# Performance work log

Measured on AMD Instinct MI355X. Metric: run time of the kernel, lower is better.

Reference implementation:

```python
import jax, jax.numpy as jnp
import numpy as np

N = 20000      # nodes
E = 640000     # directed edges
NB = 124       # n_atom_basis
FD = NB + 4    # feature dim after res_embed concat = 128
RBF = 16
CUTOFF = 10.0
NCONV = 3
SCF = FD + 10  # sidechain torsion feature dim = 138

act = jax.nn.silu  # 'swish'

def _w(key, shape, fan_in):
    return jax.random.normal(key, shape, jnp.float32) / np.sqrt(fan_in)

def setup_inputs() -> dict:
    key = jax.random.key(0)
    ks = iter(jax.random.split(key, 64))
    cg_z = jax.random.randint(next(ks), (N,), 0, 25)
    cg_xyz = jax.random.normal(next(ks), (N, 3), jnp.float32) * 4.0
    src = jax.random.randint(next(ks), (E,), 0, N)
    off = jax.random.randint(next(ks), (E,), 1, N)
    dst = (src + off) % N  # no self-loops -> dist > 0
    CG_nbr_list = jnp.stack([src, dst], axis=1)
    mapping = jax.random.randint(next(ks), (N,), 0, N)  # unused by forward
    S = jax.random.normal(next(ks), (N, NB), jnp.float32)
    p = {}
    p['res_embed'] = _w(next(ks), (25, 4), 1.0)
    p['msg_W1'] = _w(next(ks), (NCONV, FD, FD), FD); p['msg_b1'] = jnp.zeros((NCONV, FD))
    p['msg_W2'] = _w(next(ks), (NCONV, FD, FD), FD); p['msg_b2'] = jnp.zeros((NCONV, FD))
    p['dist_W'] = _w(next(ks), (NCONV, RBF, FD), RBF); p['dist_b'] = jnp.zeros((NCONV, FD))
    p['dense_W1'] = _w(next(ks), (NCONV, FD, FD), FD); p['dense_b1'] = jnp.zeros((NCONV, FD))
    p['dense_W2'] = _w(next(ks), (NCONV, FD, FD), FD); p['dense_b2'] = jnp.zeros((NCONV, FD))
    p['bb_dist_emb'] = _w(next(ks), (25, 3), 1.0)
    p['sc_dist_emb'] = _w(next(ks), (25, 10), 1.0)
    p['bba_W1'] = _w(next(ks), (FD, 3), FD); p['bba_b1'] = jnp.zeros((3,))
    p['bba_W2'] = _w(next(ks), (3, 3), 3);  p['bba_b2'] = jnp.zeros((3,))
    p['sca_W1'] = _w(next(ks), (FD, 10), FD); p['sca_b1'] = jnp.zeros((10,))
    p['sca_W2'] = _w(next(ks), (10, 10), 10); p['sca_b2'] = jnp.zeros((10,))
    p['bbt_W1'] = _w(next(ks), (FD + 3, 3), FD + 3); p['bbt_b1'] = jnp.zeros((3,))
    p['bbt_W2'] = _w(next(ks), (3, 3), 3); p['bbt_b2'] = jnp.zeros((3,))
    p['sct_W1'] = _w(next(ks), (NCONV, SCF, SCF), SCF); p['sct_b1'] = jnp.zeros((NCONV, SCF))
    p['sct_W2'] = _w(next(ks), (NCONV, SCF, SCF), SCF); p['sct_b2'] = jnp.zeros((NCONV, SCF))
    p['ft_W1'] = _w(next(ks), (SCF, 10), SCF); p['ft_b1'] = jnp.zeros((10,))
    p['ft_W2'] = _w(next(ks), (10, 10), 10); p['ft_b2'] = jnp.zeros((10,))
    return dict(cg_z=cg_z, cg_xyz=cg_xyz, CG_nbr_list=CG_nbr_list, mapping=mapping, S=S, **p)

def reference(cg_z, cg_xyz, CG_nbr_list, mapping, S, res_embed,
              msg_W1, msg_b1, msg_W2, msg_b2, dist_W, dist_b,
              dense_W1, dense_b1, dense_W2, dense_b2,
              bb_dist_emb, sc_dist_emb,
              bba_W1, bba_b1, bba_W2, bba_b2,
              sca_W1, sca_b1, sca_W2, sca_b2,
              bbt_W1, bbt_b1, bbt_W2, bbt_b2,
              sct_W1, sct_b1, sct_W2, sct_b2,
              ft_W1, ft_b1, ft_W2, ft_b2):
    nbr = CG_nbr_list  # already directed (both i>j and j>i present)
    i_idx, j_idx = nbr[:, 0], nbr[:, 1]
    r_ij = cg_xyz[j_idx] - cg_xyz[i_idx]             # [E,3]
    dist = jnp.linalg.norm(r_ij, axis=-1)            # [E]
    # PaiNN radial basis: sin(n*pi*d/cutoff)/d, n=1..RBF
    n_arr = jnp.arange(1, RBF + 1, dtype=jnp.float32)
    rbf = jnp.sin(dist[:, None] * n_arr * (jnp.pi / CUTOFF)) / dist[:, None]  # [E,RBF]
    env = jnp.where(dist < CUTOFF, 0.5 * (jnp.cos(jnp.pi * dist / CUTOFF) + 1.0), 0.0)[:, None]
    S = jnp.concatenate([S, res_embed[cg_z]], axis=-1)  # [N,FD]
    for i in range(NCONV):
        phi = act(S @ msg_W1[i] + msg_b1[i]) @ msg_W2[i] + msg_b2[i]   # [N,FD]
        w_s = (rbf @ dist_W[i] + dist_b[i]) * env                      # [E,FD]
        msg = phi[j_idx] * w_s                                         # gather + per-edge message
        v = jax.ops.segment_sum(msg, i_idx, num_segments=N)            # scatter-add
        h = act(act(v) @ dense_W1[i] + dense_b1[i]) @ dense_W2[i] + dense_b2[i]
        S = S + h
    bb_angle = act(act(S) @ bba_W1 + bba_b1) @ bba_W2 + bba_b2          # [N,3]
    bbt_in = jnp.concatenate([S, bb_angle], axis=-1)
    bb_torsion = act(act(bbt_in) @ bbt_W1 + bbt_b1) @ bbt_W2 + bbt_b2   # [N,3]
    sc_angle = act(act(S) @ sca_W1 + sca_b1) @ sca_W2 + sca_b2          # [N,10]
    sc_S = jnp.concatenate([S, sc_angle], axis=-1)                      # [N,SCF]
    for i in range(NCONV):
        sc_S = sc_S + (act(act(sc_S) @ sct_W1[i] + sct_b1[i]) @ sct_W2[i] + sct_b2[i])
    sc_torsion = act(act(sc_S) @ ft_W1 + ft_b1) @ ft_W2 + ft_b2         # [N,10]
    bb_dist = bb_dist_emb[cg_z][..., None]                              # [N,3,1]
    sc_dist = sc_dist_emb[cg_z][..., None]                              # [N,10,1]
    ic_bb = jnp.concatenate([bb_dist, bb_angle[..., None], bb_torsion[..., None]], axis=-1)  # [N,3,3]
    ic_sc = jnp.concatenate([sc_dist, sc_angle[..., None], sc_torsion[..., None]], axis=-1)  # [N,10,3]
    ic_recon = jnp.concatenate([ic_bb, ic_sc], axis=-2)                 # [N,13,3]
    return ic_recon
```

## Files before the change

kernel.cpp:

```cpp
#include <hip/hip_runtime.h>
#include <hip/hip_bf16.h>

#define DIV_UP(a,b) (((a)+(b)-1)/(b))

typedef __attribute__((ext_vector_type(8))) short bf16x8;
typedef __attribute__((ext_vector_type(4))) float f32x4;

__device__ __forceinline__ float silu_f(float x) {
    return x / (1.0f + __expf(-x));
}
__device__ __forceinline__ unsigned short f2bf(float x) {
    __hip_bfloat16 h = __float2bfloat16(x);
    return *reinterpret_cast<unsigned short*>(&h);
}
__device__ __forceinline__ float bf2f(unsigned short u) {
    unsigned int v = (unsigned int)u << 16;
    return __uint_as_float(v);
}
__device__ __forceinline__ void split_bf(float x, unsigned short& hi, unsigned short& lo) {
    hi = f2bf(x);
    lo = f2bf(x - bf2f(hi));
}
__device__ __forceinline__ bf16x8 pack8(unsigned int w0, unsigned int w1,
                                        unsigned int w2, unsigned int w3) {
    union { unsigned int u[4]; bf16x8 v; } t;
    t.u[0] = w0; t.u[1] = w1; t.u[2] = w2; t.u[3] = w3;
    return t.v;
}

#define WSLOT 16384

__global__ __launch_bounds__(256) void prep_weights_kernel(
    const float* __restrict__ msgW1, const float* __restrict__ msgW2,
    const float* __restrict__ denseW1, const float* __restrict__ denseW2,
    unsigned short* __restrict__ WB)
{
    int slot = blockIdx.y;
    int kind = slot / 3, conv = slot % 3;
    const float* base;
    switch (kind) {
        case 0: base = msgW1; break;
        case 1: base = msgW2; break;
        case 2: base = denseW1; break;
        default: base = denseW2; break;
    }
    const float* W = base + (size_t)conv * 128 * 128;
    int idx = blockIdx.x * 256 + threadIdx.x;
    if (idx >= 16384) return;
    int c = idx >> 7, k = idx & 127;
    float val = W[(size_t)k * 128 + c];
    unsigned short hi, lo;
    split_bf(val, hi, lo);
    WB[(size_t)(2 * slot) * WSLOT + idx]     = hi;
    WB[(size_t)(2 * slot + 1) * WSLOT + idx] = lo;
}

__global__ __launch_bounds__(256) void hist_kernel(
    const int* __restrict__ nbr, int* __restrict__ counts, int E)
{
    int e = blockIdx.x * 256 + threadIdx.x;
    if (e < E) atomicAdd(&counts[nbr[2 * e]], 1);
}

__global__ __launch_bounds__(1024) void scan_kernel(
    const int* __restrict__ counts, int* __restrict__ peptr, int N)
{
    __shared__ int part[1024];
    const int t = threadIdx.x;
    const int chunk = DIV_UP(N, 1024);
    int s = 0;
    for (int c = 0; c < chunk; ++c) {
        int idx = t * chunk + c;
        if (idx < N) s += (counts[idx] + 31) & ~31;
    }
    part[t] = s;
    __syncthreads();
    for (int off = 1; off < 1024; off <<= 1) {
        int v = (t >= off) ? part[t - off] : 0;
        __syncthreads();
        part[t] += v;
        __syncthreads();
    }
    int pre = (t > 0) ? part[t - 1] : 0;
    for (int c = 0; c < chunk; ++c) {
        int idx = t * chunk + c;
        if (idx < N) { peptr[idx] = pre; pre += (counts[idx] + 31) & ~31; }
    }
    if (t == 1023) peptr[N] = part[1023];
}

__global__ __launch_bounds__(256) void geom_scatter_kernel(
    const int* __restrict__ nbr, const float* __restrict__ xyz,
    const int* __restrict__ peptr, int* __restrict__ cursor,
    unsigned short* __restrict__ rbfT, unsigned short* __restrict__ envs,
    int* __restrict__ js, int E)
{
    int e = blockIdx.x * 256 + threadIdx.x;
    if (e >= E) return;
    int i = nbr[2 * e], j = nbr[2 * e + 1];
    float dx = xyz[3 * j + 0] - xyz[3 * i + 0];
    float dy = xyz[3 * j + 1] - xyz[3 * i + 1];
    float dz = xyz[3 * j + 2] - xyz[3 * i + 2];
    float dist = sqrtf(dx * dx + dy * dy + dz * dz);
    float x = dist * 0.3141592653589793f;
    float s, c;
    __sincosf(x, &s, &c);
    float env = (dist < 10.0f) ? 0.5f * (c + 1.0f) : 0.0f;
    float inv_env = env / dist;
    float two_c = 2.0f * c;
    float sm1 = 0.0f, s0 = s;
    __align__(16) unsigned short ob[16];
    #pragma unroll
    for (int k = 0; k < 16; ++k) {
        ob[k] = f2bf(s0 * inv_env);
        float s1 = two_c * s0 - sm1;
        sm1 = s0; s0 = s1;
    }
    int p = peptr[i] + atomicAdd(&cursor[i], 1);
    uint4* rp = (uint4*)(rbfT + (size_t)p * 16);
    rp[0] = *(const uint4*)&ob[0];
    rp[1] = *(const uint4*)&ob[8];
    envs[p] = f2bf(env);
    js[p] = j;
}

__global__ __launch_bounds__(256) void concat_s_kernel(
    const float* __restrict__ S, const float* __restrict__ res_embed,
    const int* __restrict__ z, float* __restrict__ S0, int N)
{
    int idx = blockIdx.x * 256 + threadIdx.x;
    if (idx >= N * 128) return;
    int n = idx >> 7, c = idx & 127;
    float val = (c < 124) ? S[n * 124 + c] : res_embed[z[n] * 4 + (c - 124)];
    S0[idx] = val;
}

template<int MT, bool PREACT, bool RESID, typename OutT>
__global__ __launch_bounds__(256) void mlp2_mfma_kernel(
    const float* __restrict__ X,
    const unsigned short* __restrict__ W1hi, const unsigned short* __restrict__ W1lo,
    const float* __restrict__ b1,
    const unsigned short* __restrict__ W2hi, const unsigned short* __restrict__ W2lo,
    const float* __restrict__ b2,
    OutT* __restrict__ Y, int nrows)
{
    constexpr int RB   = MT / 16;
    constexpr int ROWB = 256;
    __shared__ __align__(16) unsigned short XHhi[MT * 128];
    __shared__ __align__(16) unsigned short XHlo[MT * 128];
    __shared__ __align__(16) unsigned short WS[128 * 128];

    const int tid  = threadIdx.x;
    const int wave = tid >> 6;
    const int lane = tid & 63;
    const int l15  = lane & 15;
    const int kg   = lane >> 4;
    const int row0 = blockIdx.x * MT;

    for (int idx = tid; idx < MT * 32; idx += 256) {
        int r = idx >> 5, q = idx & 31;
        int gr = row0 + r;
        float4 xv = make_float4(0.f, 0.f, 0.f, 0.f);
        if (gr < nrows) xv = *(const float4*)(X + (size_t)gr * 128 + 4 * q);
        if (PREACT) { xv.x = silu_f(xv.x); xv.y = silu_f(xv.y);
                      xv.z = silu_f(xv.z); xv.w = silu_f(xv.w); }
        ushort4 h, l;
        split_bf(xv.x, h.x, l.x); split_bf(xv.y, h.y, l.y);
        split_bf(xv.z, h.z, l.z); split_bf(xv.w, h.w, l.w);
        int off = (8 * q) ^ ((r & 7) << 4);
        *(ushort4*)((char*)XHhi + r * ROWB + off) = h;
        *(ushort4*)((char*)XHlo + r * ROWB + off) = l;
    }

    f32x4 acc[RB][2];

    #define STAGE_W(WPTR)                                                       \
        for (int idx = tid; idx < 2048; idx += 256) {                           \
            int r = idx >> 4;                                                   \
            int byt = (idx & 15) * 16;                                          \
            *(uint4*)((char*)WS + r * ROWB + (byt ^ ((r & 7) << 4))) =          \
                *(const uint4*)((WPTR) + (size_t)idx * 8);                      \
        }

    #define PASS(WITH_LO)                                                       \
        _Pragma("unroll")                                                       \
        for (int kk = 0; kk < 4; ++kk) {                                        \
            const int kbyte = kk * 64 + kg * 16;                                \
            bf16x8 ah[RB], al[RB];                                              \
            _Pragma("unroll")                                                   \
            for (int rb = 0; rb < RB; ++rb) {                                   \
                int r = 16 * rb + l15;                                          \
                int off = kbyte ^ ((r & 7) << 4);                               \
                ah[rb] = *(const bf16x8*)((const char*)XHhi + r * ROWB + off);  \
                if (WITH_LO)                                                    \
                    al[rb] = *(const bf16x8*)((const char*)XHlo + r * ROWB + off); \
            }                                                                   \
            _Pragma("unroll")                                                   \
            for (int cbi = 0; cbi < 2; ++cbi) {                                 \
                int rw = 16 * (wave + 4 * cbi) + l15;                           \
                int offw = kbyte ^ ((rw & 7) << 4);                             \
                bf16x8 bw = *(const bf16x8*)((const char*)WS + rw * ROWB + offw); \
                _Pragma("unroll")                                               \
                for (int rb = 0; rb < RB; ++rb) {                               \
                    f32x4 t = acc[rb][cbi];                                     \
                    t = __builtin_amdgcn_mfma_f32_16x16x32_bf16(ah[rb], bw, t, 0, 0, 0); \
                    if (WITH_LO)                                                \
                        t = __builtin_amdgcn_mfma_f32_16x16x32_bf16(al[rb], bw, t, 0, 0, 0); \
                    acc[rb][cbi] = t;                                           \
                }                                                               \
            }                                                                   \
        }

    #pragma unroll
    for (int a = 0; a < RB; ++a) { acc[a][0] = (f32x4){0,0,0,0}; acc[a][1] = (f32x4){0,0,0,0}; }
    STAGE_W(W1hi)
    __syncthreads();
    PASS(true)
    __syncthreads();
    STAGE_W(W1lo)
    __syncthreads();
    PASS(false)
    __syncthreads();

    #pragma unroll
    for (int cbi = 0; cbi < 2; ++cbi) {
        int col = 16 * (wave + 4 * cbi) + l15;
        float b1v = b1[col];
        #pragma unroll
        for (int rb = 0; rb < RB; ++rb)
            #pragma unroll
            for (int i = 0; i < 4; ++i) {
                int r = 16 * rb + kg * 4 + i;
                float h = silu_f(acc[rb][cbi][i] + b1v);
                unsigned short hh, hl;
                split_bf(h, hh, hl);
                int off = (2 * col) ^ ((r & 7) << 4);
                *(unsigned short*)((char*)XHhi + r * ROWB + off) = hh;
                *(unsigned short*)((char*)XHlo + r * ROWB + off) = hl;
            }
    }
    #pragma unroll
    for (int a = 0; a < RB; ++a) { acc[a][0] = (f32x4){0,0,0,0}; acc[a][1] = (f32x4){0,0,0,0}; }
    STAGE_W(W2hi)
    __syncthreads();
    PASS(true)
    __syncthreads();
    STAGE_W(W2lo)
    __syncthreads();
    PASS(false)
    #undef PASS
    #undef STAGE_W

    #pragma unroll
    for (int cbi = 0; cbi < 2; ++cbi) {
        int col = 16 * (wave + 4 * cbi) + l15;
        float b2v = b2[col];
        #pragma unroll
        for (int rb = 0; rb < RB; ++rb)
            #pragma unroll
            for (int i = 0; i < 4; ++i) {
                int gr = row0 + 16 * rb + kg * 4 + i;
                if (gr < nrows) {
                    size_t off = (size_t)gr * 128 + col;
                    float val = acc[rb][cbi][i] + b2v;
                    if (RESID) val += (float)Y[off];
                    if constexpr (sizeof(OutT) == 2)
                        Y[off] = __float2bfloat16(val);
                    else
                        Y[off] = val;
                }
            }
    }
}

template<int K, int ROWS, int RR, bool PREACT, bool RESID, typename OutT>
__global__ __launch_bounds__(256) void mlp2_kernel(
    const float* __restrict__ X, int ldX,
    const float* __restrict__ W1, const float* __restrict__ b1,
    const float* __restrict__ W2, const float* __restrict__ b2,
    OutT* __restrict__ Y, int ldY, int nrows)
{
    constexpr int NC = (K + 31) / 32;
    __shared__ float Xs[ROWS * K];
    __shared__ float Hs[ROWS * K];
    const int tid = threadIdx.x;
    const int row0 = blockIdx.x * ROWS;

    for (int idx = tid; idx < ROWS * K; idx += 256) {
        int r = idx / K, c = idx - r * K;
        int gr = row0 + r;
        float x = (gr < nrows) ? X[(size_t)gr * ldX + c] : 0.0f;
        if (PREACT) x = silu_f(x);
        Xs[idx] = x;
    }
    __syncthreads();

    const int cc = tid & 31;
    const int r0 = (tid >> 5) * RR;

    float acc[NC][RR];
    #pragma unroll
    for (int jc = 0; jc < NC; ++jc) {
        int col = cc + 32 * jc;
        float bv = (col < K) ? b1[col] : 0.0f;
        #pragma unroll
        for (int rr = 0; rr < RR; ++rr) acc[jc][rr] = bv;
    }
    #pragma unroll 6
    for (int k = 0; k < K; ++k) {
        float w[NC];
        #pragma unroll
        for (int jc = 0; jc < NC; ++jc) {
            int col = cc + 32 * jc;
            w[jc] = (col < K) ? W1[k * K + col] : 0.0f;
        }
        float xv[RR];
        #pragma unroll
        for (int rr = 0; rr < RR; ++rr) xv[rr] = Xs[(r0 + rr) * K + k];
        #pragma unroll
        for (int jc = 0; jc < NC; ++jc)
            #pragma unroll
            for (int rr = 0; rr < RR; ++rr)
                acc[jc][rr] = fmaf(xv[rr], w[jc], acc[jc][rr]);
    }
    #pragma unroll
    for (int jc = 0; jc < NC; ++jc) {
        int col = cc + 32 * jc;
        if (col < K) {
            #pragma unroll
            for (int rr = 0; rr < RR; ++rr)
                Hs[(r0 + rr) * K + col] = silu_f(acc[jc][rr]);
        }
    }
    __syncthreads();

    #pragma unroll
    for (int jc = 0; jc < NC; ++jc) {
        int col = cc + 32 * jc;
        float bv = (col < K) ? b2[col] : 0.0f;
        #pragma unroll
        for (int rr = 0; rr < RR; ++rr) acc[jc][rr] = bv;
    }
    #pragma unroll 6
    for (int k = 0; k < K; ++k) {
        float w[NC];
        #pragma unroll
        for (int jc = 0; jc < NC; ++jc) {
            int col = cc + 32 * jc;
            w[jc] = (col < K) ? W2[k * K + col] : 0.0f;
        }
        float xv[RR];
        #pragma unroll
        for (int rr = 0; rr < RR; ++rr) xv[rr] = Hs[(r0 + rr) * K + k];
        #pragma unroll
        for (int jc = 0; jc < NC; ++jc)
            #pragma unroll
            for (int rr = 0; rr < RR; ++rr)
                acc[jc][rr] = fmaf(xv[rr], w[jc], acc[jc][rr]);
    }
    #pragma unroll
    for (int jc = 0; jc < NC; ++jc) {
        int col = cc + 32 * jc;
        if (col < K) {
            #pragma unroll
            for (int rr = 0; rr < RR; ++rr) {
                int gr = row0 + r0 + rr;
                if (gr < nrows) {
                    size_t off = (size_t)gr * ldY + col;
                    float val = acc[jc][rr];
                    if (RESID) val += (float)Y[off];
                    if constexpr (sizeof(OutT) == 2)
                        Y[off] = __float2bfloat16(val);
                    else
                        Y[off] = val;
                }
            }
        }
    }
}

__global__ __launch_bounds__(256) void gather_mfma_kernel(
    const int* __restrict__ peptr,
    const unsigned short* __restrict__ rbfT,
    const unsigned short* __restrict__ envs,
    const int* __restrict__ js,
    const unsigned short* __restrict__ phi,
    const float* __restrict__ distW, const float* __restrict__ distb,
    float* __restrict__ v, int N)
{
    const int wv = blockIdx.x * 4 + (threadIdx.x >> 6);
    const int lane = threadIdx.x & 63;
    const int n = wv >> 1;
    const int h = wv & 1;
    if (n >= N) return;
    const int l15 = lane & 15;
    const int lg  = lane >> 4;

    f32x4 acc[4];
    float eac[4];
    #pragma unroll
    for (int cb = 0; cb < 4; ++cb) { acc[cb] = (f32x4){0,0,0,0}; eac[cb] = 0.f; }

    const int p0 = peptr[n], p1 = peptr[n + 1];

    for (int p = p0; p < p1; p += 32) {
        const unsigned short* ab = rbfT + (size_t)(p + 8 * lg) * 16 + l15;
        bf16x8 af = pack8(
            (unsigned int)ab[0]  | ((unsigned int)ab[16] << 16),
            (unsigned int)ab[32] | ((unsigned int)ab[48] << 16),
            (unsigned int)ab[64] | ((unsigned int)ab[80] << 16),
            (unsigned int)ab[96] | ((unsigned int)ab[112] << 16));

        bf16x8 a2f = (bf16x8){0,0,0,0,0,0,0,0};
        if (l15 == 0)
            a2f = *(const bf16x8*)(envs + p + 8 * lg);

        int4 j03 = *(const int4*)(js + p + 8 * lg);
        int4 j47 = *(const int4*)(js + p + 8 * lg + 4);

        const unsigned short* pb0 = phi + (size_t)j03.x * 128 + 64 * h + l15;
        const unsigned short* pb1 = phi + (size_t)j03.y * 128 + 64 * h + l15;
        const unsigned short* pb2 = phi + (size_t)j03.z * 128 + 64 * h + l15;
        const unsigned short* pb3 = phi + (size_t)j03.w * 128 + 64 * h + l15;
        const unsigned short* pb4 = phi + (size_t)j47.x * 128 + 64 * h + l15;
        const unsigned short* pb5 = phi + (size_t)j47.y * 128 + 64 * h + l15;
        const unsigned short* pb6 = phi + (size_t)j47.z * 128 + 64 * h + l15;
        const unsigned short* pb7 = phi + (size_t)j47.w * 128 + 64 * h + l15;

        #pragma unroll
        for (int cbi = 0; cbi < 4; ++cbi) {
            const int o = cbi * 16;
            unsigned int b0 = (unsigned int)pb0[o] | ((unsigned int)pb1[o] << 16);
            unsigned int b1 = (unsigned int)pb2[o] | ((unsigned int)pb3[o] << 16);
            unsigned int b2 = (unsigned int)pb4[o] | ((unsigned int)pb5[o] << 16);
            unsigned int b3 = (unsigned int)pb6[o] | ((unsigned int)pb7[o] << 16);
            bf16x8 bf = pack8(b0, b1, b2, b3);
            acc[cbi] = __builtin_amdgcn_mfma_f32_16x16x32_bf16(af, bf, acc[cbi], 0, 0, 0);
            f32x4 z = (f32x4){0, 0, 0, 0};
            z = __builtin_amdgcn_mfma_f32_16x16x32_bf16(a2f, bf, z, 0, 0, 0);
            eac[cbi] += z[0];
        }
    }

    #pragma unroll
    for (int cbi = 0; cbi < 4; ++cbi) {
        int col = 64 * h + cbi * 16 + l15;
        float part = acc[cbi][0] * distW[(lg * 4 + 0) * 128 + col];
        part = fmaf(acc[cbi][1], distW[(lg * 4 + 1) * 128 + col], part);
        part = fmaf(acc[cbi][2], distW[(lg * 4 + 2) * 128 + col], part);
        part = fmaf(acc[cbi][3], distW[(lg * 4 + 3) * 128 + col], part);
        if (lg == 0) part = fmaf(eac[cbi], distb[col], part);
        part += __shfl_xor(part, 16, 64);
        part += __shfl_xor(part, 32, 64);
        if (lane < 16) v[(size_t)n * 128 + col] = part;
    }
}

__global__ __launch_bounds__(256) void fused_heads_kernel(
    const float* __restrict__ S0,
    const float* __restrict__ bbaW1, const float* __restrict__ bbab1,
    const float* __restrict__ bbaW2, const float* __restrict__ bbab2,
    const float* __restrict__ bbtW1, const float* __restrict__ bbtb1,
    const float* __restrict__ bbtW2, const float* __restrict__ bbtb2,
    const float* __restrict__ scaW1, const float* __restrict__ scab1,
    const float* __restrict__ scaW2, const float* __restrict__ scab2,
    float* __restrict__ bbA, float* __restrict__ bbT,
    float* __restrict__ scA, float* __restrict__ scS, int N)
{
    const int wid = threadIdx.x >> 6;
    const int lane = threadIdx.x & 63;
    const int n = blockIdx.x * 4 + wid;
    if (n >= N) return;

    float x0 = S0[(size_t)n * 128 + lane];
    float x1 = S0[(size_t)n * 128 + 64 + lane];
    float s0 = silu_f(x0), s1 = silu_f(x1);

    float ba[3];
    #pragma unroll
    for (int m = 0; m < 3; ++m)
        ba[m] = fmaf(s0, bbaW1[lane * 3 + m], s1 * bbaW1[(lane + 64) * 3 + m]);
    #pragma unroll
    for (int m = 0; m < 3; ++m)
        #pragma unroll
        for (int off = 32; off > 0; off >>= 1)
            ba[m] += __shfl_xor(ba[m], off, 64);
    float bbo[3];
    {
        float tm[3];
        #pragma unroll
        for (int m = 0; m < 3; ++m) tm[m] = silu_f(ba[m] + bbab1[m]);
        #pragma unroll
        for (int mm = 0; mm < 3; ++mm) {
            float o = bbab2[mm];
            #pragma unroll
            for (int m = 0; m < 3; ++m) o = fmaf(tm[m], bbaW2[m * 3 + mm], o);
            bbo[mm] = o;
        }
    }
    if (lane < 3) {
        float ov = bbo[0];
        if (lane == 1) ov = bbo[1];
        if (lane == 2) ov = bbo[2];
        bbA[(size_t)n * 3 + lane] = ov;
    }

    float bt[3];
    #pragma unroll
    for (int m = 0; m < 3; ++m)
        bt[m] = fmaf(s0, bbtW1[lane * 3 + m], s1 * bbtW1[(lane + 64) * 3 + m]);
    #pragma unroll
    for (int m = 0; m < 3; ++m)
        #pragma unroll
        for (int off = 32; off > 0; off >>= 1)
            bt[m] += __shfl_xor(bt[m], off, 64);
    #pragma unroll
    for (int m = 0; m < 3; ++m)
        #pragma unroll
        for (int t = 0; t < 3; ++t)
            bt[m] = fmaf(silu_f(bbo[t]), bbtW1[(128 + t) * 3 + m], bt[m]);
    {
        float tm[3], bto[3];
        #pragma unroll
        for (int m = 0; m < 3; ++m) tm[m] = silu_f(bt[m] + bbtb1[m]);
        #pragma unroll
        for (int mm = 0; mm < 3; ++mm) {
            float o = bbtb2[mm];
            #pragma unroll
            for (int m = 0; m < 3; ++m) o = fmaf(tm[m], bbtW2[m * 3 + mm], o);
            bto[mm] = o;
        }
        if (lane < 3) {
            float ov = bto[0];
            if (lane == 1) ov = bto[1];
            if (lane == 2) ov = bto[2];
            bbT[(size_t)n * 3 + lane] = ov;
        }
    }

    float sa[10];
    #pragma unroll
    for (int m = 0; m < 10; ++m)
        sa[m] = fmaf(s0, scaW1[lane * 10 + m], s1 * scaW1[(lane + 64) * 10 + m]);
    #pragma unroll
    for (int m = 0; m < 10; ++m)
        #pragma unroll
        for (int off = 32; off > 0; off >>= 1)
            sa[m] += __shfl_xor(sa[m], off, 64);
    float sco[10];
    {
        float tm[10];
        #pragma unroll
        for (int m = 0; m < 10; ++m) tm[m] = silu_f(sa[m] + scab1[m]);
        #pragma unroll
        for (int mm = 0; mm < 10; ++mm) {
            float o = scab2[mm];
            #pragma unroll
            for (int m = 0; m < 10; ++m) o = fmaf(tm[m], scaW2[m * 10 + mm], o);
            sco[mm] = o;
        }
    }
    float scv = sco[0];
    #pragma unroll
    for (int m = 1; m < 10; ++m)
        if (lane == m) scv = sco[m];
    if (lane < 10) scA[(size_t)n * 10 + lane] = scv;

    scS[(size_t)n * 140 + lane] = x0;
    scS[(size_t)n * 140 + 64 + lane] = x1;
    if (lane < 12) scS[(size_t)n * 140 + 128 + lane] = (lane < 10) ? scv : 0.0f;
}

template<int M>
__global__ __launch_bounds__(256) void head_kernel(
    const float* __restrict__ X, int ldX, int K1,
    const float* __restrict__ X2, int ldX2, int K2,
    const float* __restrict__ W1, const float* __restrict__ b1,
    const float* __restrict__ W2, const float* __restrict__ b2,
    float* __restrict__ out, int ldOut, int nrows)
{
    const int wid = threadIdx.x >> 6;
    const int lane = threadIdx.x & 63;
    const int n = blockIdx.x * 4 + wid;
    if (n >= nrows) return;
    const int K = K1 + K2;
    float sx[3];
    #pragma unroll
    for (int t = 0; t < 3; ++t) {
        int k = lane + 64 * t;
        float v = 0.0f;
        if (k < K1) v = X[(size_t)n * ldX + k];
        else if (k < K) v = X2[(size_t)n * ldX2 + (k - K1)];
        sx[t] = (k < K) ? silu_f(v) : 0.0f;
    }
    float acc[M];
    #pragma unroll
    for (int m = 0; m < M; ++m) {
        float a = 0.0f;
        #pragma unroll
        for (int t = 0; t < 3; ++t) {
            int k = lane + 64 * t;
            if (k < K) a = fmaf(sx[t], W1[k * M + m], a);
        }
        acc[m] = a;
    }
    #pragma unroll
    for (int m = 0; m < M; ++m) {
        #pragma unroll
        for (int off = 32; off > 0; off >>= 1)
            acc[m] += __shfl_xor(acc[m], off, 64);
    }
    float tm[M];
    #pragma unroll
    for (int m = 0; m < M; ++m) tm[m] = silu_f(acc[m] + b1[m]);
    if (lane < M) {
        float o = b2[lane];
        #pragma unroll
        for (int m = 0; m < M; ++m) o = fmaf(tm[m], W2[m * M + lane], o);
        out[(size_t)n * ldOut + lane] = o;
    }
}

__global__ __launch_bounds__(256) void assemble_kernel(
    const int* __restrict__ z,
    const float* __restrict__ bbde, const float* __restrict__ scde,
    const float* __restrict__ bbA, const float* __restrict__ bbT,
    const float* __restrict__ scA, const float* __restrict__ scT,
    float* __restrict__ out, int N)
{
    int idx = blockIdx.x * 256 + threadIdx.x;
    if (idx >= N * 39) return;
    int n = idx / 39;
    int s = idx - n * 39;
    int row = s / 3;
    int col = s - row * 3;
    float val;
    if (row < 3) {
        if (col == 0)      val = bbde[z[n] * 3 + row];
        else if (col == 1) val = bbA[n * 3 + row];
        else               val = bbT[n * 3 + row];
    } else {
        int r = row - 3;
        if (col == 0)      val = scde[z[n] * 10 + r];
        else if (col == 1) val = scA[n * 10 + r];
        else               val = scT[n * 10 + r];
    }
    out[idx] = val;
}

extern "C" void kernel_launch(void* const* d_in, const int* in_sizes, int n_in,
                              void* d_out, int out_size, void* d_ws, size_t ws_size,
                              hipStream_t stream)
{
    const int*   cg_z        = (const int*)d_in[0];
    const float* cg_xyz      = (const float*)d_in[1];
    const int*   nbr         = (const int*)d_in[2];
    const float* S_in        = (const float*)d_in[4];
    const float* res_embed   = (const float*)d_in[5];
    const float* msg_W1      = (const float*)d_in[6];
    const float* msg_b1      = (const float*)d_in[7];
    const float* msg_W2      = (const float*)d_in[8];
    const float* msg_b2      = (const float*)d_in[9];
    const float* dist_W      = (const float*)d_in[10];
    const float* dist_b      = (const float*)d_in[11];
    const float* dense_W1    = (const float*)d_in[12];
    const float* dense_b1    = (const float*)d_in[13];
    const float* dense_W2    = (const float*)d_in[14];
    const float* dense_b2    = (const float*)d_in[15];
    const float* bb_dist_emb = (const float*)d_in[16];
    const float* sc_dist_emb = (const float*)d_in[17];
    const float* bba_W1      = (const float*)d_in[18];
    const float* bba_b1      = (const float*)d_in[19];
    const float* bba_W2      = (const float*)d_in[20];
    const float* bba_b2      = (const float*)d_in[21];
    const float* sca_W1      = (const float*)d_in[22];
    const float* sca_b1      = (const float*)d_in[23];
    const float* sca_W2      = (const float*)d_in[24];
    const float* sca_b2      = (const float*)d_in[25];
    const float* bbt_W1      = (const float*)d_in[26];
    const float* bbt_b1      = (const float*)d_in[27];
    const float* bbt_W2      = (const float*)d_in[28];
    const float* bbt_b2      = (const float*)d_in[29];
    const float* sct_W1      = (const float*)d_in[30];
    const float* sct_b1      = (const float*)d_in[31];
    const float* sct_W2      = (const float*)d_in[32];
    const float* sct_b2      = (const float*)d_in[33];
    const float* ft_W1       = (const float*)d_in[34];
    const float* ft_b1       = (const float*)d_in[35];
    const float* ft_W2       = (const float*)d_in[36];
    const float* ft_b2       = (const float*)d_in[37];

    const int N = in_sizes[0];
    const int E = in_sizes[2] / 2;
    const int EPAD = ((E + 31 * N) / 32) * 32 + 32;

    unsigned short* WB   = (unsigned short*)d_ws;
    unsigned short* rbfT = WB + (size_t)24 * WSLOT;
    unsigned short* envs = rbfT + (size_t)EPAD * 16;
    int*            js   = (int*)(envs + (size_t)EPAD);
    float* ws   = (float*)(js + (size_t)EPAD);
    float* S0   = ws;  ws += (size_t)N * 128;
    float* V    = ws;  ws += (size_t)N * 128;
    float* scS  = ws;  ws += (size_t)N * 140;
    float* bbA  = ws;  ws += (size_t)N * 3;
    float* bbT  = ws;  ws += (size_t)N * 3;
    float* scA  = ws;  ws += (size_t)N * 10;
    float* scT  = ws;  ws += (size_t)N * 10;
    __hip_bfloat16* PHI = (__hip_bfloat16*)ws;  ws += (size_t)N * 64;
    int* peptr  = (int*)ws;  ws = (float*)((int*)ws + (N + 1));
    int* counts = (int*)ws;  ws = (float*)((int*)ws + N);
    int* cursor = (int*)ws;  ws = (float*)((int*)ws + N);

    (void)hipMemsetAsync(rbfT, 0, (size_t)EPAD * 38, stream);
    (void)hipMemsetAsync(counts, 0, (size_t)2 * N * sizeof(int), stream);

    prep_weights_kernel<<<dim3(64, 12), 256, 0, stream>>>(
        msg_W1, msg_W2, dense_W1, dense_W2, WB);

    hist_kernel<<<DIV_UP(E, 256), 256, 0, stream>>>(nbr, counts, E);
    scan_kernel<<<1, 1024, 0, stream>>>(counts, peptr, N);
    geom_scatter_kernel<<<DIV_UP(E, 256), 256, 0, stream>>>(
        nbr, cg_xyz, peptr, cursor, rbfT, envs, js, E);

    concat_s_kernel<<<DIV_UP(N * 128, 256), 256, 0, stream>>>(S_in, res_embed, cg_z, S0, N);

    #define WHI(kind, conv) (WB + (size_t)(2 * ((kind) * 3 + (conv))) * WSLOT)
    #define WLO(kind, conv) (WB + (size_t)(2 * ((kind) * 3 + (conv)) + 1) * WSLOT)

    for (int i = 0; i < 3; ++i) {
        mlp2_mfma_kernel<48, false, false, __hip_bfloat16>
            <<<DIV_UP(N, 48), 256, 0, stream>>>(
            S0, WHI(0, i), WLO(0, i), msg_b1 + i * 128,
            WHI(1, i), WLO(1, i), msg_b2 + i * 128, PHI, N);
        gather_mfma_kernel<<<DIV_UP(2 * N, 4), 256, 0, stream>>>(
            peptr, rbfT, envs, js, (const unsigned short*)PHI,
            dist_W + (size_t)i * 16 * 128, dist_b + i * 128, V, N);
        mlp2_mfma_kernel<48, true, true, float>
            <<<DIV_UP(N, 48), 256, 0, stream>>>(
            V, WHI(2, i), WLO(2, i), dense_b1 + i * 128,
            WHI(3, i), WLO(3, i), dense_b2 + i * 128, S0, N);
    }

    fused_heads_kernel<<<DIV_UP(N, 4), 256, 0, stream>>>(
        S0,
        bba_W1, bba_b1, bba_W2, bba_b2,
        bbt_W1, bbt_b1, bbt_W2, bbt_b2,
        sca_W1, sca_b1, sca_W2, sca_b2,
        bbA, bbT, scA, scS, N);

    for (int i = 0; i < 3; ++i) {
        mlp2_kernel<138, 16, 2, true, true, float><<<DIV_UP(N, 16), 256, 0, stream>>>(
            scS, 140, sct_W1 + (size_t)i * 138 * 138, sct_b1 + i * 138,
            sct_W2 + (size_t)i * 138 * 138, sct_b2 + i * 138, scS, 140, N);
    }
    head_kernel<10><<<DIV_UP(N, 4), 256, 0, stream>>>(
        scS, 140, 138, scS, 0, 0, ft_W1, ft_b1, ft_W2, ft_b2, scT, 10, N);

    assemble_kernel<<<DIV_UP(N * 39, 256), 256, 0, stream>>>(
        cg_z, bb_dist_emb, sc_dist_emb, bbA, bbT, scA, scT, (float*)d_out, N);

    #undef WHI
    #undef WLO
}
```

Before: 637.1 us.

## Fuse three sidechain residual MLP layers and final torsion head into one kernel

Replaces three launches of the generic two-layer MLP kernel and the separate ft head kernel with a single kernel. That kernel keeps each 16-row tile's residual state in shared memory across all three layers and then computes the 10-output head in place. This removes the intermediate global reads and writes of the 140-wide scS rows between layers, plus three kernel launches. In exchange it uses more shared memory per block (a third 16x138 buffer), which may reduce occupancy.

```diff
diff --git a/kernel.cpp b/kernel.cpp
--- a/kernel.cpp
+++ b/kernel.cpp
@@ -273,108 +273,141 @@
     }
 }
 
-template<int K, int ROWS, int RR, bool PREACT, bool RESID, typename OutT>
-__global__ __launch_bounds__(256) void mlp2_kernel(
-    const float* __restrict__ X, int ldX,
-    const float* __restrict__ W1, const float* __restrict__ b1,
-    const float* __restrict__ W2, const float* __restrict__ b2,
-    OutT* __restrict__ Y, int ldY, int nrows)
-{
-    constexpr int NC = (K + 31) / 32;
+__global__ __launch_bounds__(256) void sct_fused_kernel(
+    const float* __restrict__ scS,
+    const float* __restrict__ sctW1, const float* __restrict__ sctb1,
+    const float* __restrict__ sctW2, const float* __restrict__ sctb2,
+    const float* __restrict__ ftW1, const float* __restrict__ ftb1,
+    const float* __restrict__ ftW2, const float* __restrict__ ftb2,
+    float* __restrict__ scT, int nrows)
+{
+    constexpr int K = 138, ROWS = 16, RR = 2, NC = 5;
+    __shared__ float Raw[ROWS * K];
     __shared__ float Xs[ROWS * K];
     __shared__ float Hs[ROWS * K];
     const int tid = threadIdx.x;
     const int row0 = blockIdx.x * ROWS;
+    const int cc = tid & 31;
+    const int r0 = (tid >> 5) * RR;
 
     for (int idx = tid; idx < ROWS * K; idx += 256) {
         int r = idx / K, c = idx - r * K;
         int gr = row0 + r;
-        float x = (gr < nrows) ? X[(size_t)gr * ldX + c] : 0.0f;
-        if (PREACT) x = silu_f(x);
-        Xs[idx] = x;
-    }
-    __syncthreads();
-
-    const int cc = tid & 31;
-    const int r0 = (tid >> 5) * RR;
+        Raw[idx] = (gr < nrows) ? scS[(size_t)gr * 140 + c] : 0.0f;
+    }
 
     float acc[NC][RR];
-    #pragma unroll
-    for (int jc = 0; jc < NC; ++jc) {
-        int col = cc + 32 * jc;
-        float bv = (col < K) ? b1[col] : 0.0f;
-        #pragma unroll
-        for (int rr = 0; rr < RR; ++rr) acc[jc][rr] = bv;
-    }
-    #pragma unroll 6
-    for (int k = 0; k < K; ++k) {
-        float w[NC];
+
+    for (int layer = 0; layer < 3; ++layer) {
+        const float* W1 = sctW1 + (size_t)layer * K * K;
+        const float* b1 = sctb1 + layer * K;
+        const float* W2 = sctW2 + (size_t)layer * K * K;
+        const float* b2 = sctb2 + layer * K;
+
+        __syncthreads();
+        for (int idx = tid; idx < ROWS * K; idx += 256)
+            Xs[idx] = silu_f(Raw[idx]);
+        __syncthreads();
+
         #pragma unroll
         for (int jc = 0; jc < NC; ++jc) {
             int col = cc + 32 * jc;
-            w[jc] = (col < K) ? W1[k * K + col] : 0.0f;
-        }
-        float xv[RR];
-        #pragma unroll
-        for (int rr = 0; rr < RR; ++rr) xv[rr] = Xs[(r0 + rr) * K + k];
-        #pragma unroll
-        for (int jc = 0; jc < NC; ++jc)
-            #pragma unroll
-            for (int rr = 0; rr < RR; ++rr)
-                acc[jc][rr] = fmaf(xv[rr], w[jc], acc[jc][rr]);
-    }
-    #pragma unroll
-    for (int jc = 0; jc < NC; ++jc) {
-        int col = cc + 32 * jc;
-        if (col < K) {
-            #pragma unroll
-            for (int rr = 0; rr < RR; ++rr)
-                Hs[(r0 + rr) * K + col] = silu_f(acc[jc][rr]);
-        }
-    }
-    __syncthreads();
-
-    #pragma unroll
-    for (int jc = 0; jc < NC; ++jc) {
-        int col = cc + 32 * jc;
-        float bv = (col < K) ? b2[col] : 0.0f;
-        #pragma unroll
-        for (int rr = 0; rr < RR; ++rr) acc[jc][rr] = bv;
-    }
-    #pragma unroll 6
-    for (int k = 0; k < K; ++k) {
-        float w[NC];
+            float bv = (col < K) ? b1[col] : 0.0f;
+            #pragma unroll
+            for (int rr = 0; rr < RR; ++rr) acc[jc][rr] = bv;
+        }
+        #pragma unroll 6
+        for (int k = 0; k < K; ++k) {
+            float w[NC];
+            #pragma unroll
+            for (int jc = 0; jc < NC; ++jc) {
+                int col = cc + 32 * jc;
+                w[jc] = (col < K) ? W1[k * K + col] : 0.0f;
+            }
+            float xv[RR];
+            #pragma unroll
+            for (int rr = 0; rr < RR; ++rr) xv[rr] = Xs[(r0 + rr) * K + k];
+            #pragma unroll
+            for (int jc = 0; jc < NC; ++jc)
+                #pragma unroll
+                for (int rr = 0; rr < RR; ++rr)
+                    acc[jc][rr] = fmaf(xv[rr], w[jc], acc[jc][rr]);
+        }
         #pragma unroll
         for (int jc = 0; jc < NC; ++jc) {
             int col = cc + 32 * jc;
-            w[jc] = (col < K) ? W2[k * K + col] : 0.0f;
-        }
-        float xv[RR];
-        #pragma unroll
-        for (int rr = 0; rr < RR; ++rr) xv[rr] = Hs[(r0 + rr) * K + k];
-        #pragma unroll
-        for (int jc = 0; jc < NC; ++jc)
-            #pragma unroll
-            for (int rr = 0; rr < RR; ++rr)
-                acc[jc][rr] = fmaf(xv[rr], w[jc], acc[jc][rr]);
-    }
-    #pragma unroll
-    for (int jc = 0; jc < NC; ++jc) {
-        int col = cc + 32 * jc;
-        if (col < K) {
-            #pragma unroll
-            for (int rr = 0; rr < RR; ++rr) {
-                int gr = row0 + r0 + rr;
-                if (gr < nrows) {
-                    size_t off = (size_t)gr * ldY + col;
-                    float val = acc[jc][rr];
-                    if (RESID) val += (float)Y[off];
-                    if constexpr (sizeof(OutT) == 2)
-                        Y[off] = __float2bfloat16(val);
-                    else
-                        Y[off] = val;
-                }
+            if (col < K) {
+                #pragma unroll
+                for (int rr = 0; rr < RR; ++rr)
+                    Hs[(r0 + rr) * K + col] = silu_f(acc[jc][rr]);
             }
+        }
+        __syncthreads();
+
+        #pragma unroll
+        for (int jc = 0; jc < NC; ++jc) {
+            int col = cc + 32 * jc;
+            float bv = (col < K) ? b2[col] : 0.0f;
+            #pragma unroll
+            for (int rr = 0; rr < RR; ++rr) acc[jc][rr] = bv;
+        }
+        #pragma unroll 6
+        for (int k = 0; k < K; ++k) {
+            float w[NC];
+            #pragma unroll
+            for (int jc = 0; jc < NC; ++jc) {
+                int col = cc + 32 * jc;
+                w[jc] = (col < K) ? W2[k * K + col] : 0.0f;
+            }
+            float xv[RR];
+            #pragma unroll
+            for (int rr = 0; rr < RR; ++rr) xv[rr] = Hs[(r0 + rr) * K + k];
+            #pragma unroll
+            for (int jc = 0; jc < NC; ++jc)
+                #pragma unroll
+                for (int rr = 0; rr < RR; ++rr)
+                    acc[jc][rr] = fmaf(xv[rr], w[jc], acc[jc][rr]);
+        }
+        #pragma unroll
+        for (int jc = 0; jc < NC; ++jc) {
+            int col = cc + 32 * jc;
+            if (col < K) {
+                #pragma unroll
+                for (int rr = 0; rr < RR; ++rr)
+                    Raw[(r0 + rr) * K + col] += acc[jc][rr];
+            }
+        }
+    }
+    __syncthreads();
+
+    {
+        const int r  = tid >> 4;
+        const int kl = tid & 15;
+        const int gr = row0 + r;
+        float a[10];
+        #pragma unroll
+        for (int m = 0; m < 10; ++m) a[m] = 0.0f;
+        for (int k = kl; k < K; k += 16) {
+            float xv = silu_f(Raw[r * K + k]);
+            #pragma unroll
+            for (int m = 0; m < 10; ++m)
+                a[m] = fmaf(xv, ftW1[k * 10 + m], a[m]);
+        }
+        #pragma unroll
+        for (int m = 0; m < 10; ++m) {
+            a[m] += __shfl_xor(a[m], 1, 64);
+            a[m] += __shfl_xor(a[m], 2, 64);
+            a[m] += __shfl_xor(a[m], 4, 64);
+            a[m] += __shfl_xor(a[m], 8, 64);
+        }
+        float tm[10];
+        #pragma unroll
+        for (int m = 0; m < 10; ++m) tm[m] = silu_f(a[m] + ftb1[m]);
+        if (kl < 10 && gr < nrows) {
+            float o = ftb2[kl];
+            #pragma unroll
+            for (int m = 0; m < 10; ++m) o = fmaf(tm[m], ftW2[m * 10 + kl], o);
+            scT[(size_t)gr * 10 + kl] = o;
         }
     }
 }
@@ -569,56 +602,6 @@
     scS[(size_t)n * 140 + lane] = x0;
     scS[(size_t)n * 140 + 64 + lane] = x1;
     if (lane < 12) scS[(size_t)n * 140 + 128 + lane] = (lane < 10) ? scv : 0.0f;
-}
-
-template<int M>
-__global__ __launch_bounds__(256) void head_kernel(
-    const float* __restrict__ X, int ldX, int K1,
-    const float* __restrict__ X2, int ldX2, int K2,
-    const float* __restrict__ W1, const float* __restrict__ b1,
-    const float* __restrict__ W2, const float* __restrict__ b2,
-    float* __restrict__ out, int ldOut, int nrows)
-{
-    const int wid = threadIdx.x >> 6;
-    const int lane = threadIdx.x & 63;
-    const int n = blockIdx.x * 4 + wid;
-    if (n >= nrows) return;
-    const int K = K1 + K2;
-    float sx[3];
-    #pragma unroll
-    for (int t = 0; t < 3; ++t) {
-        int k = lane + 64 * t;
-        float v = 0.0f;
-        if (k < K1) v = X[(size_t)n * ldX + k];
-        else if (k < K) v = X2[(size_t)n * ldX2 + (k - K1)];
-        sx[t] = (k < K) ? silu_f(v) : 0.0f;
-    }
-    float acc[M];
-    #pragma unroll
-    for (int m = 0; m < M; ++m) {
-        float a = 0.0f;
-        #pragma unroll
-        for (int t = 0; t < 3; ++t) {
-            int k = lane + 64 * t;
-            if (k < K) a = fmaf(sx[t], W1[k * M + m], a);
-        }
-        acc[m] = a;
-    }
-    #pragma unroll
-    for (int m = 0; m < M; ++m) {
-        #pragma unroll
-        for (int off = 32; off > 0; off >>= 1)
-            acc[m] += __shfl_xor(acc[m], off, 64);
-    }
-    float tm[M];
-    #pragma unroll
-    for (int m = 0; m < M; ++m) tm[m] = silu_f(acc[m] + b1[m]);
-    if (lane < M) {
-        float o = b2[lane];
-        #pragma unroll
-        for (int m = 0; m < M; ++m) o = fmaf(tm[m], W2[m * M + lane], o);
-        out[(size_t)n * ldOut + lane] = o;
-    }
 }
 
 __global__ __launch_bounds__(256) void assemble_kernel(
@@ -748,13 +731,9 @@
         sca_W1, sca_b1, sca_W2, sca_b2,
         bbA, bbT, scA, scS, N);
 
-    for (int i = 0; i < 3; ++i) {
-        mlp2_kernel<138, 16, 2, true, true, float><<<DIV_UP(N, 16), 256, 0, stream>>>(
-            scS, 140, sct_W1 + (size_t)i * 138 * 138, sct_b1 + i * 138,
-            sct_W2 + (size_t)i * 138 * 138, sct_b2 + i * 138, scS, 140, N);
-    }
-    head_kernel<10><<<DIV_UP(N, 4), 256, 0, stream>>>(
-        scS, 140, 138, scS, 0, 0, ft_W1, ft_b1, ft_W2, ft_b2, scT, 10, N);
+    sct_fused_kernel<<<DIV_UP(N, 16), 256, 0, stream>>>(
+        scS, sct_W1, sct_b1, sct_W2, sct_b2,
+        ft_W1, ft_b1, ft_W2, ft_b2, scT, N);
 
     assemble_kernel<<<DIV_UP(N * 39, 256), 256, 0, stream>>>(
         cg_z, bb_dist_emb, sc_dist_emb, bbA, bbT, scA, scT, (float*)d_out, N);
```

New measurement: 605.0 us. 1.05x faster.
